# Kernel optimization log

Hardware: AMD Instinct MI355X
Metric: run time of the kernel (lower is better)

The kernel has to match this reference:

```python
import jax, jax.numpy as jnp
import numpy as np

N_TYPES = 4
NEG_SLOPE = 0.01


def _conv(x, row, col, edge_type, edge_weight, W, b):
    # x: [N, d_in], W: [4, d_in, d_out], b: [d_out]
    N = x.shape[0]
    # in-degree based symmetric normalization (deg counted on col, as in source)
    deg = jax.ops.segment_sum(jnp.ones(col.shape[0], dtype=x.dtype), col, num_segments=N)
    deg_inv_sqrt = jnp.where(deg > 0, deg ** -0.5, jnp.zeros((), x.dtype))
    norm = deg_inv_sqrt[row] * deg_inv_sqrt[col] * edge_weight  # [E]
    # project all nodes by each of the 4 relation weights, then gather per edge
    # (equivalent to per-edge bmm x[col] @ W[edge_type], but avoids [E,d,d])
    xw = jnp.einsum('ni,tio->tno', x, W)          # [4, N, d_out]
    x_j = xw[edge_type, col] * norm[:, None]      # [E, d_out]
    out = jax.ops.segment_sum(x_j, row, num_segments=N) + b  # [N, d_out]
    # dropout omitted (eval mode / deterministic reference)
    return jax.nn.leaky_relu(out, negative_slope=NEG_SLOPE)


def setup_inputs() -> dict:
    key = jax.random.key(0)
    ks = jax.random.split(key, 10)
    N, d, E = 50000, 128, 625000
    x = jax.random.normal(ks[0], (N, d), dtype=jnp.float32)
    edge_index = jax.random.randint(ks[1], (2, E), 0, N, dtype=jnp.int64 if jax.config.jax_enable_x64 else jnp.int32)
    edge_type = jax.random.randint(ks[2], (E,), 0, N_TYPES)
    edge_attr = jax.random.uniform(ks[3], (E,), dtype=jnp.float32)
    # xavier_uniform for (4, d, d): gain=1, bound = sqrt(6/(d+d))
    bound = float(np.sqrt(6.0 / (d + d)))
    W1 = jax.random.uniform(ks[4], (N_TYPES, d, d), minval=-bound, maxval=bound, dtype=jnp.float32)
    W2 = jax.random.uniform(ks[5], (N_TYPES, d, d), minval=-bound, maxval=bound, dtype=jnp.float32)
    W3 = jax.random.uniform(ks[6], (N_TYPES, d, d), minval=-bound, maxval=bound, dtype=jnp.float32)
    b1 = jnp.zeros((d,), jnp.float32)
    b2 = jnp.zeros((d,), jnp.float32)
    b3 = jnp.zeros((d,), jnp.float32)
    return {"x": x, "edge_index": edge_index, "edge_type": edge_type, "edge_attr": edge_attr,
            "W1": W1, "b1": b1, "W2": W2, "b2": b2, "W3": W3, "b3": b3}


def reference(x, edge_index, edge_type, edge_attr, W1, b1, W2, b2, W3, b3):
    row, col = edge_index[0], edge_index[1]
    z1 = _conv(x, row, col, edge_type, edge_attr, W1, b1)
    z2 = _conv(z1, row, col, edge_type, edge_attr, W2, b2)
    z3 = _conv(z2, row, col, edge_type, edge_attr, W3, b3)
    return (x + z1 + z2 + z3) / 4
```

## Files before the change

kernel.cpp:

```cpp
#include <hip/hip_runtime.h>

#define DIM 128
#define SLOTS 64

typedef __attribute__((ext_vector_type(8))) short bf16x8;
typedef __attribute__((ext_vector_type(4))) float f32x4;
typedef __attribute__((ext_vector_type(2))) float f32x2;
typedef unsigned short u16;
typedef unsigned int u32;
typedef unsigned long long u64;

__device__ __forceinline__ float bf2f(u32 u) {
    return __builtin_bit_cast(float, u << 16);
}
__device__ __forceinline__ u16 f2bf(float f) {
    u32 u = __builtin_bit_cast(u32, f);
    u = (u + 0x7FFFu + ((u >> 16) & 1u)) >> 16;
    return (u16)u;
}
__device__ __forceinline__ u32 pack2bf(float a, float b) {
    return (u32)f2bf(a) | ((u32)f2bf(b) << 16);
}


__global__ __launch_bounds__(256) void k_setup(const int* __restrict__ row, const int* __restrict__ col,
                                               const int* __restrict__ et, const float* __restrict__ ew,
                                               int E, int* __restrict__ deg, int* __restrict__ fill,
                                               u64* __restrict__ ep,
                                               const float* __restrict__ x, u16* __restrict__ xb, int nx4,
                                               const float* __restrict__ W1, const float* __restrict__ W2,
                                               const float* __restrict__ W3,
                                               u16* __restrict__ Wt1, u16* __restrict__ Wt2,
                                               u16* __restrict__ Wt3, int nEb, int nXb) {
    int b = blockIdx.x, tid = threadIdx.x;
    if (b < nEb) {
        int e0 = (b * 256 + tid) * 4;
        #pragma unroll
        for (int i = 0; i < 4; i++) {
            int e = e0 + i;
            if (e < E) {
                int r = row[e], c = col[e];
                atomicAdd(&deg[c], 1);
                int pos = atomicAdd(&fill[r], 1);
                if (pos < SLOTS)
                    ep[(size_t)r * SLOTS + pos] =
                        ((u64)__builtin_bit_cast(u32, ew[e]) << 32) | (u32)((c << 8) | et[e]);
            }
        }
    } else if (b < nEb + nXb) {
        int i = (b - nEb) * 256 + tid;
        if (i < nx4) {
            float4 v = ((const float4*)x)[i];
            ushort4 o;
            o.x = f2bf(v.x); o.y = f2bf(v.y); o.z = f2bf(v.z); o.w = f2bf(v.w);
            ((ushort4*)xb)[i] = o;
        }
    } else {
        int b2 = b - nEb - nXb;
        const float* W = b2 < 256 ? W1 : (b2 < 512 ? W2 : W3);
        u16* Wt = b2 < 256 ? Wt1 : (b2 < 512 ? Wt2 : Wt3);
        int o = (b2 & 255) * 256 + tid;
        int chunk = o >> 10;
        int c = (o >> 3) & 127;
        int k = chunk * 8 + (o & 7);
        Wt[o] = f2bf(W[(k >> 7) * 16384 + (k & 127) * 128 + c]);
    }
}


__global__ __launch_bounds__(256) void k_norm(const int* __restrict__ fill,
                                              const int* __restrict__ deg,
                                              u64* __restrict__ ep, int N) {
    int wid = threadIdx.x >> 6, lane = threadIdx.x & 63;
    int n = blockIdx.x * 4 + wid;
    if (n >= N) return;
    int cnt = fill[n]; if (cnt > SLOTS) cnt = SLOTS;
    int padded = (cnt + 7) & ~7;
    int dgn = deg[n];
    float dn = dgn > 0 ? rsqrtf((float)dgn) : 0.f;
    u64* eb = ep + (size_t)n * SLOTS;
    if (lane < cnt) {
        u64 q = eb[lane];
        u32 lo = (u32)q;
        int dgc = deg[lo >> 8];
        float dc = dgc > 0 ? rsqrtf((float)dgc) : 0.f;
        float wgt = __builtin_bit_cast(float, (u32)(q >> 32)) * dn * dc;
        eb[lane] = ((u64)__builtin_bit_cast(u32, wgt) << 32) | lo;
    } else if (lane < padded) {
        eb[lane] = 0;
    }
}


template <int MODE>
__global__ __launch_bounds__(1024, 2) void k_layer(const u16* __restrict__ src,
                                                   const int* __restrict__ fill,
                                                   const u64* __restrict__ ep,
                                                   const u16* __restrict__ Wt,
                                                   const float* __restrict__ bias,
                                                   const float* __restrict__ x0,
                                                   const u16* __restrict__ z1b,
                                                   const u16* __restrict__ z2b,
                                                   float* __restrict__ outf,
                                                   u16* __restrict__ outb, int N) {
    __shared__ u16 sA[16 * 512];
    int tid = threadIdx.x, wid = tid >> 6, lane = tid & 63;
    int n0 = blockIdx.x * 16;
    int n = n0 + wid;

    f32x2 a0 = {0.f, 0.f}, a1 = {0.f, 0.f}, a2 = {0.f, 0.f}, a3 = {0.f, 0.f};
    int cnt = 0;
    if (n < N) {
        cnt = fill[n];
        if (cnt > SLOTS) cnt = SLOTS;
    }
    u64 myq = ep[(size_t)n * SLOTS + lane];
    u32 mylo = (u32)myq;
    u32 mywu = (u32)(myq >> 32);
    const char* srcc = (const char*)src;

#define RL(x, i_) ((u32)__builtin_amdgcn_readlane((int)(x), (i_)))

#define EDGE(lo_, wu_, v_) { \
        float w_  = __builtin_bit_cast(float, (u32)(wu_)); \
        f32x2 vv_; \
        vv_[0] = __builtin_bit_cast(float, (v_) << 16); \
        vv_[1] = __builtin_bit_cast(float, (v_) & 0xFFFF0000u); \
        u32 t_ = (u32)(lo_) & 3u; \
        float w0_ = t_ == 0u ? w_ : 0.f; \
        float w1_ = t_ == 1u ? w_ : 0.f; \
        float w2_ = t_ == 2u ? w_ : 0.f; \
        float w3_ = t_ == 3u ? w_ : 0.f; \
        a0 = __builtin_elementwise_fma(vv_, (f32x2){w0_, w0_}, a0); \
        a1 = __builtin_elementwise_fma(vv_, (f32x2){w1_, w1_}, a1); \
        a2 = __builtin_elementwise_fma(vv_, (f32x2){w2_, w2_}, a2); \
        a3 = __builtin_elementwise_fma(vv_, (f32x2){w3_, w3_}, a3); }

    for (int j = 0; j < cnt; j += 8) {
        u32 lo[8], wu[8], v[8];
        #pragma unroll
        for (int i = 0; i < 8; i++) {
            lo[i] = RL(mylo, j + i);
            wu[i] = RL(mywu, j + i);
        }
        #pragma unroll
        for (int i = 0; i < 8; i++) {
            const u32* rowp = (const u32*)(srcc + (lo[i] & 0xFFFFFF00u));
            v[i] = rowp[lane];
        }
        #pragma unroll
        for (int i = 0; i < 8; i++)
            EDGE(lo[i], wu[i], v[i]);
    }
#undef EDGE
#undef RL

    {
        u32 X = (u32)((wid & 7) << 4);
        char* base = (char*)sA + wid * 1024;
        *(u32*)(base + ((lane * 4 + 0  ) ^ X)) = pack2bf(a0[0], a0[1]);
        *(u32*)(base + ((lane * 4 + 256) ^ X)) = pack2bf(a1[0], a1[1]);
        *(u32*)(base + ((lane * 4 + 512) ^ X)) = pack2bf(a2[0], a2[1]);
        *(u32*)(base + ((lane * 4 + 768) ^ X)) = pack2bf(a3[0], a3[1]);
    }
    __syncthreads();

    if (wid < 8) {
        int lr = lane & 15, lk = lane >> 4;
        u32 X = (u32)((lr & 7) << 4);
        const char* ab = (const char*)sA + lr * 1024;
        const u16* bb = Wt + lk * 1024 + (wid * 16 + lr) * 8;
        f32x4 acc = {};
        #pragma unroll
        for (int ks = 0; ks < 16; ks++) {
            bf16x8 af = *(const bf16x8*)(ab + ((ks * 64 + lk * 16) ^ X));
            bf16x8 bfv = *(const bf16x8*)(bb + ks * 4096);
            acc = __builtin_amdgcn_mfma_f32_16x16x32_bf16(af, bfv, acc, 0, 0, 0);
        }

        int colg = wid * 16 + lr;
        float bv = bias[colg];
        #pragma unroll
        for (int r = 0; r < 4; r++) {
            int nn = n0 + lk * 4 + r;
            if (nn < N) {
                size_t idx = (size_t)nn * DIM + colg;
                float v = acc[r] + bv;
                v = v > 0.f ? v : 0.01f * v;
                if (MODE == 1)
                    outf[idx] = 0.25f * (x0[idx] + bf2f(z1b[idx]) + bf2f(z2b[idx]) + v);
                else
                    outb[idx] = f2bf(v);
            }
        }
    }
}


extern "C" void kernel_launch(void* const* d_in, const int* in_sizes, int n_in,
                              void* d_out, int out_size, void* d_ws, size_t ws_size,
                              hipStream_t stream) {
    const float* x     = (const float*)d_in[0];
    const int*   eidx  = (const int*)d_in[1];
    const int*   etype = (const int*)d_in[2];
    const float* eattr = (const float*)d_in[3];
    const float* W1 = (const float*)d_in[4];
    const float* b1 = (const float*)d_in[5];
    const float* W2 = (const float*)d_in[6];
    const float* b2 = (const float*)d_in[7];
    const float* W3 = (const float*)d_in[8];
    const float* b3 = (const float*)d_in[9];

    const int E = in_sizes[2];
    const int N = in_sizes[0] / DIM;
    const int* row = eidx;
    const int* col = eidx + E;

    char* w = (char*)d_ws;
    size_t off = 0;
    auto alloc = [&](size_t bytes) { size_t o = off; off = (off + bytes + 255) & ~255ULL; return o; };
    size_t deg_off = alloc((size_t)N * 4);
    int*   deg  = (int*)(w + deg_off);
    int*   fill = (int*)(w + alloc((size_t)N * 4));
    size_t zero_bytes = off - deg_off;
    u64*   ep   = (u64*)(w + alloc((size_t)N * SLOTS * 8));
    u16*   xb   = (u16*)(w + alloc((size_t)N * DIM * 2));
    u16*   z1b  = (u16*)(w + alloc((size_t)N * DIM * 2));
    u16*   z2b  = (u16*)(w + alloc((size_t)N * DIM * 2));
    u16*   Wt1  = (u16*)(w + alloc(65536 * 2));
    u16*   Wt2  = (u16*)(w + alloc(65536 * 2));
    u16*   Wt3  = (u16*)(w + alloc(65536 * 2));

    hipMemsetAsync(deg, 0, zero_bytes, stream);

    int nx4 = N * DIM / 4;
    int nEb = (E + 1023) / 1024;
    int nXb = (nx4 + 255) / 256;

    k_setup<<<nEb + nXb + 768, 256, 0, stream>>>(row, col, etype, eattr, E, deg, fill, ep,
                                                 x, xb, nx4, W1, W2, W3, Wt1, Wt2, Wt3, nEb, nXb);
    k_norm<<<(N + 3) / 4, 256, 0, stream>>>(fill, deg, ep, N);

    int grid = (N + 15) / 16;
    k_layer<0><<<grid, 1024, 0, stream>>>(xb,  fill, ep, Wt1, b1, nullptr, nullptr, nullptr, nullptr, z1b, N);
    k_layer<0><<<grid, 1024, 0, stream>>>(z1b, fill, ep, Wt2, b2, nullptr, nullptr, nullptr, nullptr, z2b, N);
    k_layer<1><<<grid, 1024, 0, stream>>>(z2b, fill, ep, Wt3, b3, x, z1b, z2b, (float*)d_out, nullptr, N);
}
```

Baseline: 232.6 us.

## Compute in-degree via shared-memory histograms instead of global atomics

Removes the global atomicAdd on deg[col] from the edge setup kernel. In-degree is now counted by 32 blocks, each building an LDS histogram over one quarter of the node range for one eighth of the edges. A small reduction kernel then sums the partial counts and stores the precomputed deg^-1/2 for k_norm to read. Each block reads its full eighth of col, so col is read four times, and the change adds two extra launches and an only 32-block histogram stage.

```diff
diff --git a/kernel.cpp b/kernel.cpp
--- a/kernel.cpp
+++ b/kernel.cpp
@@ -23,9 +23,45 @@
 }
 
 
+__global__ __launch_bounds__(1024) void k_hist(const int* __restrict__ col, int E,
+                                               int* __restrict__ part, int N) {
+    __shared__ int hist[12544];
+    int b = blockIdx.x;
+    int range = b >> 3;
+    int chunk = b & 7;
+    int quarter = (N + 3) >> 2;
+    int base = range * quarter;
+    int hn = N - base; if (hn > quarter) hn = quarter;
+    for (int i = threadIdx.x; i < hn; i += 1024) hist[i] = 0;
+    __syncthreads();
+    int e0 = (int)((long long)chunk * E / 8);
+    int e1 = (int)((long long)(chunk + 1) * E / 8);
+    for (int e = e0 + threadIdx.x; e < e1; e += 1024) {
+        int c = col[e] - base;
+        if ((u32)c < (u32)hn) atomicAdd(&hist[c], 1);
+    }
+    __syncthreads();
+    int* dst = part + (size_t)b * quarter;
+    for (int i = threadIdx.x; i < hn; i += 1024) dst[i] = hist[i];
+}
+
+__global__ void k_dis2(const int* __restrict__ part, float* __restrict__ dis, int N) {
+    int i = blockIdx.x * 256 + threadIdx.x;
+    if (i >= N) return;
+    int quarter = (N + 3) >> 2;
+    int range = i / quarter;
+    int il = i - range * quarter;
+    const int* p = part + ((size_t)range * 8) * quarter + il;
+    int s = 0;
+    #pragma unroll
+    for (int b = 0; b < 8; b++) s += p[(size_t)b * quarter];
+    dis[i] = s > 0 ? rsqrtf((float)s) : 0.f;
+}
+
+
 __global__ __launch_bounds__(256) void k_setup(const int* __restrict__ row, const int* __restrict__ col,
                                                const int* __restrict__ et, const float* __restrict__ ew,
-                                               int E, int* __restrict__ deg, int* __restrict__ fill,
+                                               int E, int* __restrict__ fill,
                                                u64* __restrict__ ep,
                                                const float* __restrict__ x, u16* __restrict__ xb, int nx4,
                                                const float* __restrict__ W1, const float* __restrict__ W2,
@@ -40,7 +76,6 @@
             int e = e0 + i;
             if (e < E) {
                 int r = row[e], c = col[e];
-                atomicAdd(&deg[c], 1);
                 int pos = atomicAdd(&fill[r], 1);
                 if (pos < SLOTS)
                     ep[(size_t)r * SLOTS + pos] =
@@ -69,22 +104,19 @@
 
 
 __global__ __launch_bounds__(256) void k_norm(const int* __restrict__ fill,
-                                              const int* __restrict__ deg,
+                                              const float* __restrict__ dis,
                                               u64* __restrict__ ep, int N) {
     int wid = threadIdx.x >> 6, lane = threadIdx.x & 63;
     int n = blockIdx.x * 4 + wid;
     if (n >= N) return;
     int cnt = fill[n]; if (cnt > SLOTS) cnt = SLOTS;
     int padded = (cnt + 7) & ~7;
-    int dgn = deg[n];
-    float dn = dgn > 0 ? rsqrtf((float)dgn) : 0.f;
+    float dn = dis[n];
     u64* eb = ep + (size_t)n * SLOTS;
     if (lane < cnt) {
         u64 q = eb[lane];
         u32 lo = (u32)q;
-        int dgc = deg[lo >> 8];
-        float dc = dgc > 0 ? rsqrtf((float)dgc) : 0.f;
-        float wgt = __builtin_bit_cast(float, (u32)(q >> 32)) * dn * dc;
+        float wgt = __builtin_bit_cast(float, (u32)(q >> 32)) * dn * dis[lo >> 8];
         eb[lane] = ((u64)__builtin_bit_cast(u32, wgt) << 32) | lo;
     } else if (lane < padded) {
         eb[lane] = 0;
@@ -219,10 +251,10 @@
     char* w = (char*)d_ws;
     size_t off = 0;
     auto alloc = [&](size_t bytes) { size_t o = off; off = (off + bytes + 255) & ~255ULL; return o; };
-    size_t deg_off = alloc((size_t)N * 4);
-    int*   deg  = (int*)(w + deg_off);
     int*   fill = (int*)(w + alloc((size_t)N * 4));
-    size_t zero_bytes = off - deg_off;
+    float* dis  = (float*)(w + alloc((size_t)N * 4));
+    int    quarter = (N + 3) >> 2;
+    int*   part = (int*)(w + alloc((size_t)32 * quarter * 4));
     u64*   ep   = (u64*)(w + alloc((size_t)N * SLOTS * 8));
     u16*   xb   = (u16*)(w + alloc((size_t)N * DIM * 2));
     u16*   z1b  = (u16*)(w + alloc((size_t)N * DIM * 2));
@@ -231,15 +263,17 @@
     u16*   Wt2  = (u16*)(w + alloc(65536 * 2));
     u16*   Wt3  = (u16*)(w + alloc(65536 * 2));
 
-    hipMemsetAsync(deg, 0, zero_bytes, stream);
+    hipMemsetAsync(fill, 0, (size_t)N * 4, stream);
 
     int nx4 = N * DIM / 4;
     int nEb = (E + 1023) / 1024;
     int nXb = (nx4 + 255) / 256;
 
-    k_setup<<<nEb + nXb + 768, 256, 0, stream>>>(row, col, etype, eattr, E, deg, fill, ep,
+    k_hist<<<32, 1024, 0, stream>>>(col, E, part, N);
+    k_dis2<<<(N + 255) / 256, 256, 0, stream>>>(part, dis, N);
+    k_setup<<<nEb + nXb + 768, 256, 0, stream>>>(row, col, etype, eattr, E, fill, ep,
                                                  x, xb, nx4, W1, W2, W3, Wt1, Wt2, Wt3, nEb, nXb);
-    k_norm<<<(N + 3) / 4, 256, 0, stream>>>(fill, deg, ep, N);
+    k_norm<<<(N + 3) / 4, 256, 0, stream>>>(fill, dis, ep, N);
 
     int grid = (N + 15) / 16;
     k_layer<0><<<grid, 1024, 0, stream>>>(xb,  fill, ep, Wt1, b1, nullptr, nullptr, nullptr, nullptr, z1b, N);
```

New measurement: 234.5 us. About the same (+0.8%).
